# Performance work log

Measured on AMD Instinct MI355X. Metric: run time of the kernel, lower is better.

Reference implementation:

```python
import jax, jax.numpy as jnp
import numpy as np

HIDDEN = 128
EDGE_DIM = 32
N_NODES = 50000
N_EDGES = 800000


def setup_inputs() -> dict:
    key = jax.random.key(0)
    ks = jax.random.split(key, 8)
    node_features = jax.random.normal(ks[0], (N_NODES, HIDDEN), dtype=jnp.float32)
    edge_index = jax.random.randint(ks[1], (2, N_EDGES), 0, N_NODES, dtype=jnp.int64)
    edge_attr = jax.random.normal(ks[2], (N_EDGES, EDGE_DIM), dtype=jnp.float32)
    # parameters (Linear stored as [in, out] for x @ W + b)
    s_et = 1.0 / np.sqrt(EDGE_DIM)
    W_edge = jax.random.uniform(ks[3], (EDGE_DIM, HIDDEN), jnp.float32, -s_et, s_et)
    b_edge = jnp.zeros((HIDDEN,), jnp.float32)
    s1 = 1.0 / np.sqrt(3 * HIDDEN)
    W1 = jax.random.uniform(ks[4], (3 * HIDDEN, HIDDEN), jnp.float32, -s1, s1)
    b1 = jnp.zeros((HIDDEN,), jnp.float32)
    s2 = 1.0 / np.sqrt(HIDDEN)
    W2 = jax.random.uniform(ks[5], (HIDDEN, 1), jnp.float32, -s2, s2)
    b2 = jnp.zeros((1,), jnp.float32)
    return {
        "node_features": node_features,
        "edge_attr": edge_attr,
        "W_edge": W_edge, "b_edge": b_edge,
        "W1": W1, "b1": b1, "W2": W2, "b2": b2,
        "edge_index": edge_index,
    }


def reference(node_features, edge_attr, W_edge, b_edge, W1, b1, W2, b2, edge_index):
    row, col = edge_index[0], edge_index[1]
    src = node_features[row]                 # [E, H] gather
    dst = node_features[col]                 # [E, H] gather
    edge_feat = edge_attr @ W_edge + b_edge  # [E, H]
    combined = jnp.concatenate([src, edge_feat, dst], axis=-1)  # [E, 3H]
    h = jax.nn.relu(combined @ W1 + b1)      # [E, H]
    attn = jax.nn.sigmoid(h @ W2 + b2)       # [E, 1]
    return attn
```

## Files before the change

### kernel.cpp

```cpp
#include <hip/hip_runtime.h>
#include <hip/hip_bf16.h>

#define HIDDEN   128
#define EDGE_DIM 32
#define NNODE    50000
#define NEDGE    800000
#define KSTEPS   9
#define NFRAG    8
#define LDS_KS   8

typedef __attribute__((ext_vector_type(4))) float        f32x4;
typedef __attribute__((ext_vector_type(8))) short        bf16x8;
typedef __attribute__((ext_vector_type(4))) unsigned int u32x4;

#define BPACK_USHORTS  (KSTEPS * NFRAG * 64 * 8)
#define BIAS_OFF_BYTES (BPACK_USHORTS * 2)
#define FLAG_OFF_BYTES (BIAS_OFF_BYTES + 128 * 4)
#define NODE_OFF_BYTES 74752
#define WS_NEEDED      (NODE_OFF_BYTES + NNODE * HIDDEN * 2)

__device__ __forceinline__ unsigned short f2bf(float f) {
  unsigned u = __builtin_bit_cast(unsigned, f);
  u += 0x7FFFu + ((u >> 16) & 1u);
  return (unsigned short)(u >> 16);
}

__device__ __forceinline__ unsigned cvt_pk_bf16(float a, float b) {
  union { __hip_bfloat162 h; unsigned u; } cv;
  cv.h = __float22bfloat162_rn(make_float2(a, b));
  return cv.u;
}

__device__ __forceinline__ bf16x8 pack8(f32x4 lo, f32x4 hi) {
  u32x4 u;
  u[0] = cvt_pk_bf16(lo[0], lo[1]);
  u[1] = cvt_pk_bf16(lo[2], lo[3]);
  u[2] = cvt_pk_bf16(hi[0], hi[1]);
  u[3] = cvt_pk_bf16(hi[2], hi[3]);
  return __builtin_bit_cast(bf16x8, u);
}

__device__ __forceinline__ void gload_lds16(const void* g, void* l) {
  __builtin_amdgcn_global_load_lds(
      (const __attribute__((address_space(1))) unsigned int*)g,
      (__attribute__((address_space(3))) unsigned int*)l, 16, 0, 0);
}

__global__ void setup_kernel(const float* __restrict__ W_edge,
                             const float* __restrict__ b_edge,
                             const float* __restrict__ W1,
                             const float* __restrict__ b1,
                             const void*  __restrict__ eidx,
                             unsigned short* __restrict__ Bpack,
                             float* __restrict__ bias_eff,
                             int*   __restrict__ flag64) {
  const int bid = blockIdx.x, tid = threadIdx.x;
  if (bid < 36) {
    const int pair  = bid * 2 + (tid >> 6);
    const int lane  = tid & 63;
    const int kstep = pair >> 3;
    const int f     = pair & 7;
    const int col   = f * 16 + (lane & 15);
    const int kbase = kstep * 32 + (lane >> 4) * 8;
    float vals[8];
#pragma unroll
    for (int j = 0; j < 8; ++j) {
      const int k = kbase + j;
      float val;
      if (k < 128) {
        val = W1[k * 128 + col];
      } else if (k < 256) {
        val = W1[(k + 128) * 128 + col];
      } else {
        const int kk = k - 256;
        float s = 0.f;
        for (int t = 0; t < 128; ++t)
          s = fmaf(W_edge[kk * 128 + t], W1[(128 + t) * 128 + col], s);
        val = s;
      }
      vals[j] = val;
    }
    u32x4 sv;
#pragma unroll
    for (int j = 0; j < 4; ++j)
      sv[j] = (unsigned)f2bf(vals[2 * j]) | ((unsigned)f2bf(vals[2 * j + 1]) << 16);
    *(u32x4*)(Bpack + ((kstep * NFRAG + f) * 64 + lane) * 8) = sv;
  } else {
    if (tid < 128) {
      float s = b1[tid];
      for (int t = 0; t < 128; ++t)
        s = fmaf(b_edge[t], W1[(128 + t) * 128 + tid], s);
      bias_eff[tid] = s;
    }
    if (tid == 0) {
      const unsigned* w = (const unsigned*)eidx;
      int all0 = 1;
      for (int i = 0; i < 64; ++i) all0 &= (w[2 * i + 1] == 0u) ? 1 : 0;
      *flag64 = all0;
    }
  }
}

__global__ __launch_bounds__(256) void cvt_nodes_kernel(const float* __restrict__ nodef,
                                                        unsigned short* __restrict__ nbf) {
  const int i = blockIdx.x * 256 + threadIdx.x;
  if (i >= NNODE * HIDDEN / 8) return;
  f32x4 lo = *(const f32x4*)(nodef + i * 8);
  f32x4 hi = *(const f32x4*)(nodef + i * 8 + 4);
  *(bf16x8*)(nbf + i * 8) = pack8(lo, hi);
}

__global__ __launch_bounds__(256, 2) void edge_attn_kernel(
    const unsigned short* __restrict__ nbf,
    const float* __restrict__ eattr,
    const void*  __restrict__ eidx,
    const unsigned short* __restrict__ Bpack,
    const float* __restrict__ bias_eff,
    const float* __restrict__ W2,
    const float* __restrict__ b2,
    const int*   __restrict__ flag64,
    float* __restrict__ out) {
  __shared__ unsigned short lds_b[LDS_KS * NFRAG * 64 * 8];

  const int tid   = threadIdx.x;
  const int lane  = tid & 63;
  const int wid   = tid >> 6;
  const int ebase = blockIdx.x * 128 + wid * 32;
  const int l15   = lane & 15;
  const int kg    = lane >> 4;

  const int e0 = ebase + l15;
  const int e1 = e0 + 16;

  long r0, c0, r1, c1;
  if (*flag64) {
    const long long* p = (const long long*)eidx;
    r0 = (long)p[e0];          r1 = (long)p[e1];
    c0 = (long)p[NEDGE + e0];  c1 = (long)p[NEDGE + e1];
  } else {
    const int* p = (const int*)eidx;
    r0 = p[e0];          r1 = p[e1];
    c0 = p[NEDGE + e0];  c1 = p[NEDGE + e1];
  }

  const float* pe0 = eattr + (size_t)e0 * EDGE_DIM + kg * 8;
  const float* pe1 = eattr + (size_t)e1 * EDGE_DIM + kg * 8;
  f32x4 ea0lo = *(const f32x4*)(pe0);
  f32x4 ea0hi = *(const f32x4*)(pe0 + 4);
  f32x4 ea1lo = *(const f32x4*)(pe1);
  f32x4 ea1hi = *(const f32x4*)(pe1 + 4);

  const unsigned short* ps0 = nbf + (size_t)r0 * HIDDEN + kg * 8;
  const unsigned short* ps1 = nbf + (size_t)r1 * HIDDEN + kg * 8;
  const unsigned short* pd0 = nbf + (size_t)c0 * HIDDEN + kg * 8;
  const unsigned short* pd1 = nbf + (size_t)c1 * HIDDEN + kg * 8;
  bf16x8 as0[4], as1[4], ad0[4], ad1[4];
#pragma unroll
  for (int ks = 0; ks < 4; ++ks) {
    as0[ks] = *(const bf16x8*)(ps0 + ks * 32);
    as1[ks] = *(const bf16x8*)(ps1 + ks * 32);
    ad0[ks] = *(const bf16x8*)(pd0 + ks * 32);
    ad1[ks] = *(const bf16x8*)(pd1 + ks * 32);
  }

  bf16x8 bfr8[NFRAG];
#pragma unroll
  for (int f = 0; f < NFRAG; ++f)
    bfr8[f] = *(const bf16x8*)(Bpack + ((8 * NFRAG + f) * 64 + lane) * 8);

  float w2v[NFRAG], bv[NFRAG];
#pragma unroll
  for (int f = 0; f < NFRAG; ++f) {
    w2v[f] = W2[f * 16 + l15];
    bv[f]  = bias_eff[f * 16 + l15];
  }
  const float bias2 = b2[0];

#pragma unroll
  for (int i = 0; i < 16; ++i) {
    const char* g = (const char*)Bpack + (size_t)(i * 256 + tid) * 16;
    char*       l = (char*)lds_b + (size_t)(i * 256 + wid * 64) * 16;
    gload_lds16(g, l);
  }
  __syncthreads();

  f32x4 acc[2][NFRAG];
#pragma unroll
  for (int m = 0; m < 2; ++m)
#pragma unroll
    for (int f = 0; f < NFRAG; ++f)
      acc[m][f] = (f32x4){bv[f], bv[f], bv[f], bv[f]};

#pragma unroll
  for (int ks = 0; ks < 4; ++ks) {
#pragma unroll
    for (int f = 0; f < NFRAG; ++f) {
      bf16x8 bfr = *(const bf16x8*)(lds_b + ((ks * NFRAG + f) * 64 + lane) * 8);
      acc[0][f] = __builtin_amdgcn_mfma_f32_16x16x32_bf16(as0[ks], bfr, acc[0][f], 0, 0, 0);
      acc[1][f] = __builtin_amdgcn_mfma_f32_16x16x32_bf16(as1[ks], bfr, acc[1][f], 0, 0, 0);
    }
  }
#pragma unroll
  for (int ks = 0; ks < 4; ++ks) {
#pragma unroll
    for (int f = 0; f < NFRAG; ++f) {
      bf16x8 bfr = *(const bf16x8*)(lds_b + (((ks + 4) * NFRAG + f) * 64 + lane) * 8);
      acc[0][f] = __builtin_amdgcn_mfma_f32_16x16x32_bf16(ad0[ks], bfr, acc[0][f], 0, 0, 0);
      acc[1][f] = __builtin_amdgcn_mfma_f32_16x16x32_bf16(ad1[ks], bfr, acc[1][f], 0, 0, 0);
    }
  }
  {
    bf16x8 ae0 = pack8(ea0lo, ea0hi);
    bf16x8 ae1 = pack8(ea1lo, ea1hi);
#pragma unroll
    for (int f = 0; f < NFRAG; ++f) {
      acc[0][f] = __builtin_amdgcn_mfma_f32_16x16x32_bf16(ae0, bfr8[f], acc[0][f], 0, 0, 0);
      acc[1][f] = __builtin_amdgcn_mfma_f32_16x16x32_bf16(ae1, bfr8[f], acc[1][f], 0, 0, 0);
    }
  }

  float part[2][4];
#pragma unroll
  for (int m = 0; m < 2; ++m)
#pragma unroll
    for (int r = 0; r < 4; ++r) {
      float s = 0.f;
#pragma unroll
      for (int f = 0; f < NFRAG; ++f) {
        float h = fmaxf(acc[m][f][r], 0.f);
        s = fmaf(h, w2v[f], s);
      }
      part[m][r] = s;
    }

#pragma unroll
  for (int mask = 1; mask < 16; mask <<= 1) {
#pragma unroll
    for (int m = 0; m < 2; ++m)
#pragma unroll
      for (int r = 0; r < 4; ++r)
        part[m][r] += __shfl_xor(part[m][r], mask, 64);
  }

  if (l15 == 0) {
#pragma unroll
    for (int m = 0; m < 2; ++m)
#pragma unroll
      for (int r = 0; r < 4; ++r) {
        float x = part[m][r] + bias2;
        out[ebase + m * 16 + kg * 4 + r] = 1.f / (1.f + __expf(-x));
      }
  }
}

__global__ __launch_bounds__(256) void edge_attn_kernel_fp32(
    const float* __restrict__ nodef,
    const float* __restrict__ eattr,
    const void*  __restrict__ eidx,
    const unsigned short* __restrict__ Bpack,
    const float* __restrict__ bias_eff,
    const float* __restrict__ W2,
    const float* __restrict__ b2,
    const int*   __restrict__ flag64,
    float* __restrict__ out) {
  const int lane  = threadIdx.x & 63;
  const int wid   = threadIdx.x >> 6;
  const int ebase = blockIdx.x * 128 + wid * 32;
  const int l15   = lane & 15;
  const int kg    = lane >> 4;
  const int koff  = kg * 8;
  const int e0 = ebase + l15;
  const int e1 = e0 + 16;

  long r0, c0, r1, c1;
  if (*flag64) {
    const long long* p = (const long long*)eidx;
    r0 = (long)p[e0];          r1 = (long)p[e1];
    c0 = (long)p[NEDGE + e0];  c1 = (long)p[NEDGE + e1];
  } else {
    const int* p = (const int*)eidx;
    r0 = p[e0];          r1 = p[e1];
    c0 = p[NEDGE + e0];  c1 = p[NEDGE + e1];
  }

  f32x4 acc[2][NFRAG];
#pragma unroll
  for (int m = 0; m < 2; ++m)
#pragma unroll
    for (int f = 0; f < NFRAG; ++f)
      acc[m][f] = (f32x4){0.f, 0.f, 0.f, 0.f};

#pragma unroll 1
  for (int ks = 0; ks < KSTEPS; ++ks) {
    const float *p0, *p1;
    if (ks < 4)      { p0 = nodef + r0 * HIDDEN + ks * 32;       p1 = nodef + r1 * HIDDEN + ks * 32; }
    else if (ks < 8) { p0 = nodef + c0 * HIDDEN + (ks - 4) * 32; p1 = nodef + c1 * HIDDEN + (ks - 4) * 32; }
    else             { p0 = eattr + (long)e0 * EDGE_DIM;         p1 = eattr + (long)e1 * EDGE_DIM; }

    f32x4 lo0 = *(const f32x4*)(p0 + koff);
    f32x4 hi0 = *(const f32x4*)(p0 + koff + 4);
    f32x4 lo1 = *(const f32x4*)(p1 + koff);
    f32x4 hi1 = *(const f32x4*)(p1 + koff + 4);
    bf16x8 a0 = pack8(lo0, hi0);
    bf16x8 a1 = pack8(lo1, hi1);

#pragma unroll
    for (int f = 0; f < NFRAG; ++f) {
      bf16x8 bfr = *(const bf16x8*)(Bpack + ((ks * NFRAG + f) * 64 + lane) * 8);
      acc[0][f] = __builtin_amdgcn_mfma_f32_16x16x32_bf16(a0, bfr, acc[0][f], 0, 0, 0);
      acc[1][f] = __builtin_amdgcn_mfma_f32_16x16x32_bf16(a1, bfr, acc[1][f], 0, 0, 0);
    }
  }

  float w2v[NFRAG], bv[NFRAG];
#pragma unroll
  for (int f = 0; f < NFRAG; ++f) {
    w2v[f] = W2[f * 16 + l15];
    bv[f]  = bias_eff[f * 16 + l15];
  }
  const float bias2 = b2[0];

  float part[2][4];
#pragma unroll
  for (int m = 0; m < 2; ++m)
#pragma unroll
    for (int r = 0; r < 4; ++r) {
      float s = 0.f;
#pragma unroll
      for (int f = 0; f < NFRAG; ++f) {
        float h = acc[m][f][r] + bv[f];
        h = fmaxf(h, 0.f);
        s = fmaf(h, w2v[f], s);
      }
      part[m][r] = s;
    }

#pragma unroll
  for (int mask = 1; mask < 16; mask <<= 1) {
#pragma unroll
    for (int m = 0; m < 2; ++m)
#pragma unroll
      for (int r = 0; r < 4; ++r)
        part[m][r] += __shfl_xor(part[m][r], mask, 64);
  }

  if (l15 == 0) {
#pragma unroll
    for (int m = 0; m < 2; ++m)
#pragma unroll
      for (int r = 0; r < 4; ++r) {
        float x = part[m][r] + bias2;
        out[ebase + m * 16 + kg * 4 + r] = 1.f / (1.f + __expf(-x));
      }
  }
}

extern "C" void kernel_launch(void* const* d_in, const int* in_sizes, int n_in,
                              void* d_out, int out_size, void* d_ws, size_t ws_size,
                              hipStream_t stream) {
  const float* nodef  = (const float*)d_in[0];
  const float* eattr  = (const float*)d_in[1];
  const float* W_edge = (const float*)d_in[2];
  const float* b_edge = (const float*)d_in[3];
  const float* W1     = (const float*)d_in[4];
  const float* b1     = (const float*)d_in[5];
  const float* W2     = (const float*)d_in[6];
  const float* b2     = (const float*)d_in[7];
  const void*  eidx   = d_in[8];

  unsigned short* Bpack    = (unsigned short*)d_ws;
  float*          bias_eff = (float*)((char*)d_ws + BIAS_OFF_BYTES);
  int*            flag64   = (int*)((char*)d_ws + FLAG_OFF_BYTES);
  unsigned short* nbf      = (unsigned short*)((char*)d_ws + NODE_OFF_BYTES);

  setup_kernel<<<dim3(37), dim3(128), 0, stream>>>(W_edge, b_edge, W1, b1, eidx,
                                                   Bpack, bias_eff, flag64);

  if (ws_size >= (size_t)WS_NEEDED) {
    cvt_nodes_kernel<<<dim3((NNODE * HIDDEN / 8 + 255) / 256), dim3(256), 0, stream>>>(nodef, nbf);
    edge_attn_kernel<<<dim3(NEDGE / 128), dim3(256), 0, stream>>>(
        nbf, eattr, eidx, Bpack, bias_eff, W2, b2, flag64, (float*)d_out);
  } else {
    edge_attn_kernel_fp32<<<dim3(NEDGE / 128), dim3(256), 0, stream>>>(
        nodef, eattr, eidx, Bpack, bias_eff, W2, b2, flag64, (float*)d_out);
  }
}
```

Baseline: 129.4 us.

## Make edge kernel persistent with software-pipelined index and gather prefetch

```diff
diff --git a/kernel.cpp b/kernel.cpp
--- a/kernel.cpp
+++ b/kernel.cpp
@@ -8,6 +8,8 @@
 #define KSTEPS   9
 #define NFRAG    8
 #define LDS_KS   8
+#define NGROUP   (NEDGE / 128)
+#define GRID_MAIN 512
 
 typedef __attribute__((ext_vector_type(4))) float        f32x4;
 typedef __attribute__((ext_vector_type(8))) short        bf16x8;
@@ -17,7 +19,9 @@
 #define BIAS_OFF_BYTES (BPACK_USHORTS * 2)
 #define FLAG_OFF_BYTES (BIAS_OFF_BYTES + 128 * 4)
 #define NODE_OFF_BYTES 74752
-#define WS_NEEDED      (NODE_OFF_BYTES + NNODE * HIDDEN * 2)
+#define IDX_OFF_BYTES  (NODE_OFF_BYTES + NNODE * HIDDEN * 2)
+#define WS_NEEDED      (IDX_OFF_BYTES + 2 * NEDGE * 4)
+#define WS_NEEDED_FP32 0
 
 __device__ __forceinline__ unsigned short f2bf(float f) {
   unsigned u = __builtin_bit_cast(unsigned, f);
@@ -45,6 +49,8 @@
       (const __attribute__((address_space(1))) unsigned int*)g,
       (__attribute__((address_space(3))) unsigned int*)l, 16, 0, 0);
 }
+
+#define MFMA(a, b, c) __builtin_amdgcn_mfma_f32_16x16x32_bf16((a), (b), (c), 0, 0, 0)
 
 __global__ void setup_kernel(const float* __restrict__ W_edge,
                              const float* __restrict__ b_edge,
@@ -110,71 +116,32 @@
   *(bf16x8*)(nbf + i * 8) = pack8(lo, hi);
 }
 
+__global__ __launch_bounds__(256) void cvt_idx_kernel(const void* __restrict__ eidx,
+                                                      const int* __restrict__ flag64,
+                                                      int* __restrict__ idx32) {
+  const int i = blockIdx.x * 256 + threadIdx.x;
+  if (i >= 2 * NEDGE) return;
+  if (*flag64) idx32[i] = (int)((const long long*)eidx)[i];
+  else         idx32[i] = ((const int*)eidx)[i];
+}
+
 __global__ __launch_bounds__(256, 2) void edge_attn_kernel(
     const unsigned short* __restrict__ nbf,
     const float* __restrict__ eattr,
-    const void*  __restrict__ eidx,
+    const int*   __restrict__ idx32,
     const unsigned short* __restrict__ Bpack,
     const float* __restrict__ bias_eff,
     const float* __restrict__ W2,
     const float* __restrict__ b2,
-    const int*   __restrict__ flag64,
     float* __restrict__ out) {
   __shared__ unsigned short lds_b[LDS_KS * NFRAG * 64 * 8];
 
-  const int tid   = threadIdx.x;
-  const int lane  = tid & 63;
-  const int wid   = tid >> 6;
-  const int ebase = blockIdx.x * 128 + wid * 32;
-  const int l15   = lane & 15;
-  const int kg    = lane >> 4;
-
-  const int e0 = ebase + l15;
-  const int e1 = e0 + 16;
-
-  long r0, c0, r1, c1;
-  if (*flag64) {
-    const long long* p = (const long long*)eidx;
-    r0 = (long)p[e0];          r1 = (long)p[e1];
-    c0 = (long)p[NEDGE + e0];  c1 = (long)p[NEDGE + e1];
-  } else {
-    const int* p = (const int*)eidx;
-    r0 = p[e0];          r1 = p[e1];
-    c0 = p[NEDGE + e0];  c1 = p[NEDGE + e1];
-  }
-
-  const float* pe0 = eattr + (size_t)e0 * EDGE_DIM + kg * 8;
-  const float* pe1 = eattr + (size_t)e1 * EDGE_DIM + kg * 8;
-  f32x4 ea0lo = *(const f32x4*)(pe0);
-  f32x4 ea0hi = *(const f32x4*)(pe0 + 4);
-  f32x4 ea1lo = *(const f32x4*)(pe1);
-  f32x4 ea1hi = *(const f32x4*)(pe1 + 4);
-
-  const unsigned short* ps0 = nbf + (size_t)r0 * HIDDEN + kg * 8;
-  const unsigned short* ps1 = nbf + (size_t)r1 * HIDDEN + kg * 8;
-  const unsigned short* pd0 = nbf + (size_t)c0 * HIDDEN + kg * 8;
-  const unsigned short* pd1 = nbf + (size_t)c1 * HIDDEN + kg * 8;
-  bf16x8 as0[4], as1[4], ad0[4], ad1[4];
-#pragma unroll
-  for (int ks = 0; ks < 4; ++ks) {
-    as0[ks] = *(const bf16x8*)(ps0 + ks * 32);
-    as1[ks] = *(const bf16x8*)(ps1 + ks * 32);
-    ad0[ks] = *(const bf16x8*)(pd0 + ks * 32);
-    ad1[ks] = *(const bf16x8*)(pd1 + ks * 32);
-  }
-
-  bf16x8 bfr8[NFRAG];
-#pragma unroll
-  for (int f = 0; f < NFRAG; ++f)
-    bfr8[f] = *(const bf16x8*)(Bpack + ((8 * NFRAG + f) * 64 + lane) * 8);
-
-  float w2v[NFRAG], bv[NFRAG];
-#pragma unroll
-  for (int f = 0; f < NFRAG; ++f) {
-    w2v[f] = W2[f * 16 + l15];
-    bv[f]  = bias_eff[f * 16 + l15];
-  }
-  const float bias2 = b2[0];
+  const int tid  = threadIdx.x;
+  const int lane = tid & 63;
+  const int wid  = tid >> 6;
+  const int l15  = lane & 15;
+  const int kg   = lane >> 4;
+  const int lofs = wid * 32 + l15;
 
 #pragma unroll
   for (int i = 0; i < 16; ++i) {
@@ -182,74 +149,135 @@
     char*       l = (char*)lds_b + (size_t)(i * 256 + wid * 64) * 16;
     gload_lds16(g, l);
   }
+
+  bf16x8 bfr8[NFRAG];
+#pragma unroll
+  for (int f = 0; f < NFRAG; ++f)
+    bfr8[f] = *(const bf16x8*)(Bpack + ((8 * NFRAG + f) * 64 + lane) * 8);
+  float w2v[NFRAG], bv[NFRAG];
+#pragma unroll
+  for (int f = 0; f < NFRAG; ++f) {
+    w2v[f] = W2[f * 16 + l15];
+    bv[f]  = bias_eff[f * 16 + l15];
+  }
+  const float bias2 = b2[0];
+
   __syncthreads();
 
-  f32x4 acc[2][NFRAG];
-#pragma unroll
-  for (int m = 0; m < 2; ++m)
-#pragma unroll
-    for (int f = 0; f < NFRAG; ++f)
-      acc[m][f] = (f32x4){bv[f], bv[f], bv[f], bv[f]};
-
+  int g  = blockIdx.x;
+  int eA = g * 128 + lofs;
+  int rA0 = idx32[eA],         rA1 = idx32[eA + 16];
+  int cA0 = idx32[NEDGE + eA], cA1 = idx32[NEDGE + eA + 16];
+
+  int gB = g + GRID_MAIN; if (gB >= NGROUP) gB = g;
+  int eB = gB * 128 + lofs;
+  int rB0 = idx32[eB],         rB1 = idx32[eB + 16];
+  int cB0 = idx32[NEDGE + eB], cB1 = idx32[NEDGE + eB + 16];
+
+  bf16x8 as0[4], as1[4];
 #pragma unroll
   for (int ks = 0; ks < 4; ++ks) {
-#pragma unroll
-    for (int f = 0; f < NFRAG; ++f) {
-      bf16x8 bfr = *(const bf16x8*)(lds_b + ((ks * NFRAG + f) * 64 + lane) * 8);
-      acc[0][f] = __builtin_amdgcn_mfma_f32_16x16x32_bf16(as0[ks], bfr, acc[0][f], 0, 0, 0);
-      acc[1][f] = __builtin_amdgcn_mfma_f32_16x16x32_bf16(as1[ks], bfr, acc[1][f], 0, 0, 0);
-    }
-  }
-#pragma unroll
-  for (int ks = 0; ks < 4; ++ks) {
-#pragma unroll
-    for (int f = 0; f < NFRAG; ++f) {
-      bf16x8 bfr = *(const bf16x8*)(lds_b + (((ks + 4) * NFRAG + f) * 64 + lane) * 8);
-      acc[0][f] = __builtin_amdgcn_mfma_f32_16x16x32_bf16(ad0[ks], bfr, acc[0][f], 0, 0, 0);
-      acc[1][f] = __builtin_amdgcn_mfma_f32_16x16x32_bf16(ad1[ks], bfr, acc[1][f], 0, 0, 0);
-    }
-  }
-  {
-    bf16x8 ae0 = pack8(ea0lo, ea0hi);
-    bf16x8 ae1 = pack8(ea1lo, ea1hi);
-#pragma unroll
-    for (int f = 0; f < NFRAG; ++f) {
-      acc[0][f] = __builtin_amdgcn_mfma_f32_16x16x32_bf16(ae0, bfr8[f], acc[0][f], 0, 0, 0);
-      acc[1][f] = __builtin_amdgcn_mfma_f32_16x16x32_bf16(ae1, bfr8[f], acc[1][f], 0, 0, 0);
-    }
-  }
-
-  float part[2][4];
-#pragma unroll
-  for (int m = 0; m < 2; ++m)
-#pragma unroll
-    for (int r = 0; r < 4; ++r) {
-      float s = 0.f;
+    as0[ks] = *(const bf16x8*)(nbf + (size_t)rA0 * HIDDEN + kg * 8 + ks * 32);
+    as1[ks] = *(const bf16x8*)(nbf + (size_t)rA1 * HIDDEN + kg * 8 + ks * 32);
+  }
+
+#pragma unroll 1
+  for (; g < NGROUP; g += GRID_MAIN) {
+    int gC = g + 2 * GRID_MAIN; if (gC >= NGROUP) gC = g;
+    const int eC = gC * 128 + lofs;
+    const int rC0 = idx32[eC],         rC1 = idx32[eC + 16];
+    const int cC0 = idx32[NEDGE + eC], cC1 = idx32[NEDGE + eC + 16];
+
+    bf16x8 ad0[4], ad1[4];
+#pragma unroll
+    for (int ks = 0; ks < 4; ++ks) {
+      ad0[ks] = *(const bf16x8*)(nbf + (size_t)cA0 * HIDDEN + kg * 8 + ks * 32);
+      ad1[ks] = *(const bf16x8*)(nbf + (size_t)cA1 * HIDDEN + kg * 8 + ks * 32);
+    }
+
+    const int e0 = g * 128 + lofs;
+    const float* pe0 = eattr + (size_t)e0 * EDGE_DIM + kg * 8;
+    const float* pe1 = pe0 + 16 * EDGE_DIM;
+    f32x4 ea0lo = *(const f32x4*)(pe0);
+    f32x4 ea0hi = *(const f32x4*)(pe0 + 4);
+    f32x4 ea1lo = *(const f32x4*)(pe1);
+    f32x4 ea1hi = *(const f32x4*)(pe1 + 4);
+
+    f32x4 acc[2][NFRAG];
+#pragma unroll
+    for (int m = 0; m < 2; ++m)
+#pragma unroll
+      for (int f = 0; f < NFRAG; ++f)
+        acc[m][f] = (f32x4){bv[f], bv[f], bv[f], bv[f]};
+
+#pragma unroll
+    for (int ks = 0; ks < 4; ++ks)
 #pragma unroll
       for (int f = 0; f < NFRAG; ++f) {
-        float h = fmaxf(acc[m][f][r], 0.f);
-        s = fmaf(h, w2v[f], s);
-      }
-      part[m][r] = s;
-    }
-
-#pragma unroll
-  for (int mask = 1; mask < 16; mask <<= 1) {
+        bf16x8 bfr = *(const bf16x8*)(lds_b + ((ks * NFRAG + f) * 64 + lane) * 8);
+        acc[0][f] = MFMA(as0[ks], bfr, acc[0][f]);
+        acc[1][f] = MFMA(as1[ks], bfr, acc[1][f]);
+      }
+
+#pragma unroll
+    for (int ks = 0; ks < 4; ++ks) {
+      as0[ks] = *(const bf16x8*)(nbf + (size_t)rB0 * HIDDEN + kg * 8 + ks * 32);
+      as1[ks] = *(const bf16x8*)(nbf + (size_t)rB1 * HIDDEN + kg * 8 + ks * 32);
+    }
+
+#pragma unroll
+    for (int ks = 0; ks < 4; ++ks)
+#pragma unroll
+      for (int f = 0; f < NFRAG; ++f) {
+        bf16x8 bfr = *(const bf16x8*)(lds_b + (((ks + 4) * NFRAG + f) * 64 + lane) * 8);
+        acc[0][f] = MFMA(ad0[ks], bfr, acc[0][f]);
+        acc[1][f] = MFMA(ad1[ks], bfr, acc[1][f]);
+      }
+
+    {
+      bf16x8 ae0 = pack8(ea0lo, ea0hi);
+      bf16x8 ae1 = pack8(ea1lo, ea1hi);
+#pragma unroll
+      for (int f = 0; f < NFRAG; ++f) {
+        acc[0][f] = MFMA(ae0, bfr8[f], acc[0][f]);
+        acc[1][f] = MFMA(ae1, bfr8[f], acc[1][f]);
+      }
+    }
+
+    float part[2][4];
 #pragma unroll
     for (int m = 0; m < 2; ++m)
 #pragma unroll
-      for (int r = 0; r < 4; ++r)
-        part[m][r] += __shfl_xor(part[m][r], mask, 64);
-  }
-
-  if (l15 == 0) {
-#pragma unroll
-    for (int m = 0; m < 2; ++m)
-#pragma unroll
       for (int r = 0; r < 4; ++r) {
-        float x = part[m][r] + bias2;
-        out[ebase + m * 16 + kg * 4 + r] = 1.f / (1.f + __expf(-x));
-      }
+        float s = 0.f;
+#pragma unroll
+        for (int f = 0; f < NFRAG; ++f) {
+          float h = fmaxf(acc[m][f][r], 0.f);
+          s = fmaf(h, w2v[f], s);
+        }
+        part[m][r] = s;
+      }
+#pragma unroll
+    for (int mask = 1; mask < 16; mask <<= 1)
+#pragma unroll
+      for (int m = 0; m < 2; ++m)
+#pragma unroll
+        for (int r = 0; r < 4; ++r)
+          part[m][r] += __shfl_xor(part[m][r], mask, 64);
+
+    if (l15 == 0) {
+      const int obase = g * 128 + wid * 32;
+#pragma unroll
+      for (int m = 0; m < 2; ++m)
+#pragma unroll
+        for (int r = 0; r < 4; ++r) {
+          float x = part[m][r] + bias2;
+          out[obase + m * 16 + kg * 4 + r] = 1.f / (1.f + __expf(-x));
+        }
+    }
+
+    rA0 = rB0; rA1 = rB1; cA0 = cB0; cA1 = cB1;
+    rB0 = rC0; rB1 = rC1; cB0 = cC0; cB1 = cC1;
   }
 }
 
@@ -307,8 +335,8 @@
 #pragma unroll
     for (int f = 0; f < NFRAG; ++f) {
       bf16x8 bfr = *(const bf16x8*)(Bpack + ((ks * NFRAG + f) * 64 + lane) * 8);
-      acc[0][f] = __builtin_amdgcn_mfma_f32_16x16x32_bf16(a0, bfr, acc[0][f], 0, 0, 0);
-      acc[1][f] = __builtin_amdgcn_mfma_f32_16x16x32_bf16(a1, bfr, acc[1][f], 0, 0, 0);
+      acc[0][f] = MFMA(a0, bfr, acc[0][f]);
+      acc[1][f] = MFMA(a1, bfr, acc[1][f]);
     }
   }
 
@@ -336,13 +364,12 @@
     }
 
 #pragma unroll
-  for (int mask = 1; mask < 16; mask <<= 1) {
+  for (int mask = 1; mask < 16; mask <<= 1)
 #pragma unroll
     for (int m = 0; m < 2; ++m)
 #pragma unroll
       for (int r = 0; r < 4; ++r)
         part[m][r] += __shfl_xor(part[m][r], mask, 64);
-  }
 
   if (l15 == 0) {
 #pragma unroll
@@ -372,14 +399,16 @@
   float*          bias_eff = (float*)((char*)d_ws + BIAS_OFF_BYTES);
   int*            flag64   = (int*)((char*)d_ws + FLAG_OFF_BYTES);
   unsigned short* nbf      = (unsigned short*)((char*)d_ws + NODE_OFF_BYTES);
+  int*            idx32    = (int*)((char*)d_ws + IDX_OFF_BYTES);
 
   setup_kernel<<<dim3(37), dim3(128), 0, stream>>>(W_edge, b_edge, W1, b1, eidx,
                                                    Bpack, bias_eff, flag64);
 
   if (ws_size >= (size_t)WS_NEEDED) {
+    cvt_idx_kernel<<<dim3((2 * NEDGE + 255) / 256), dim3(256), 0, stream>>>(eidx, flag64, idx32);
     cvt_nodes_kernel<<<dim3((NNODE * HIDDEN / 8 + 255) / 256), dim3(256), 0, stream>>>(nodef, nbf);
-    edge_attn_kernel<<<dim3(NEDGE / 128), dim3(256), 0, stream>>>(
-        nbf, eattr, eidx, Bpack, bias_eff, W2, b2, flag64, (float*)d_out);
+    edge_attn_kernel<<<dim3(GRID_MAIN), dim3(256), 0, stream>>>(
+        nbf, eattr, idx32, Bpack, bias_eff, W2, b2, (float*)d_out);
   } else {
     edge_attn_kernel_fp32<<<dim3(NEDGE / 128), dim3(256), 0, stream>>>(
         nodef, eattr, eidx, Bpack, bias_eff, W2, b2, flag64, (float*)d_out);
```

Result: slower. 353.1 us (+172.8%).
